# Performance work log

Hardware: AMD Instinct MI355X
Metric: run time of the kernel (lower is better)

Reference implementation:

```python
import jax, jax.numpy as jnp
import numpy as np
import math

EMBED_DIM = 768
NUM_HEADS = 12
HEAD_DIM = EMBED_DIM // NUM_HEADS
EPS = 1e-6


def setup_inputs() -> dict:
    key = jax.random.key(0)
    ks = jax.random.split(key, 9)
    T, B, N, D = 4, 4, 1024, EMBED_DIM
    s = 0.02
    return {
        "x": jax.random.normal(ks[0], (T, B, N, D), dtype=jnp.float32),
        "Wq": jax.random.normal(ks[1], (D, D), dtype=jnp.float32) * s,
        "bq": jax.random.normal(ks[2], (D,), dtype=jnp.float32) * s,
        "Wk": jax.random.normal(ks[3], (D, D), dtype=jnp.float32) * s,
        "bk": jax.random.normal(ks[4], (D,), dtype=jnp.float32) * s,
        "Wv": jax.random.normal(ks[5], (D, D), dtype=jnp.float32) * s,
        "bv": jax.random.normal(ks[6], (D,), dtype=jnp.float32) * s,
        "Wo": jax.random.normal(ks[7], (D, D), dtype=jnp.float32) * s,
        "bo": jax.random.normal(ks[8], (D,), dtype=jnp.float32) * s,
    }


def _split_heads(y, T, B, N):
    # [T,B,N,D] -> [T,B,H,N,Dh]
    return y.reshape(T, B, N, NUM_HEADS, HEAD_DIM).transpose(0, 1, 3, 2, 4)


def reference(x, Wq, bq, Wk, bk, Wv, bv, Wo, bo):
    T, B, N, D = x.shape
    # q/k/v projections (nn.Linear: x @ W^T + b)
    q = _split_heads(x @ Wq.T + bq, T, B, N)
    k = _split_heads(x @ Wk.T + bk, T, B, N)
    v = _split_heads(x @ Wv.T + bv, T, B, N)
    # scores = q k^T / sqrt(head_dim)
    scores = jnp.einsum("tbhnd,tbhmd->tbhnm", q, k) / math.sqrt(HEAD_DIM)
    # spike-form normalization: relu then L1-normalize along keys
    act = jax.nn.relu(scores)
    attn = act / (act.sum(axis=-1, keepdims=True) + EPS)
    ctx = jnp.einsum("tbhnm,tbhmd->tbhnd", attn, v)
    # merge heads: [T,B,H,N,Dh] -> [T,B,N,D]
    out = ctx.transpose(0, 1, 3, 2, 4).reshape(T, B, N, D)
    return out @ Wo.T + bo
```

## Files before the change

### kernel.cpp

```cpp
#include <hip/hip_runtime.h>
#include <hip/hip_bf16.h>
#include <cstdint>


typedef __attribute__((ext_vector_type(8))) short short8;
typedef __attribute__((ext_vector_type(4))) float float4v;
typedef __attribute__((ext_vector_type(16))) float float16v;

__device__ __forceinline__ unsigned short f2bf(float f) {
  unsigned int u = __float_as_uint(f);
  u = (u + 0x7fffu + ((u >> 16) & 1u)) >> 16;
  return (unsigned short)u;
}

__device__ __forceinline__ unsigned int pkbf(float a, float b) {
  unsigned int ua = __float_as_uint(a) + 0x8000u;
  unsigned int ub = __float_as_uint(b) + 0x8000u;
  return __builtin_amdgcn_perm(ub, ua, 0x07060302u);
}

__device__ __forceinline__ void gld_lds16(const void* g, void* lds) {
  __builtin_amdgcn_global_load_lds(
      (__attribute__((address_space(1))) void*)(uintptr_t)g,
      (__attribute__((address_space(3))) void*)(uint32_t)(uintptr_t)lds,
      16, 0, 0);
}

__global__ __launch_bounds__(256) void cast_all(
    const float* __restrict__ x,  const float* __restrict__ Wq,
    const float* __restrict__ Wk, const float* __restrict__ Wv,
    const float* __restrict__ Wo, unsigned short* __restrict__ XBF,
    unsigned short* __restrict__ WQKV, unsigned short* __restrict__ WOb) {
  const int bid = blockIdx.x;
  const float* src;
  unsigned short* dst;
  int i;
  if (bid < 12288) {
    src = x; dst = XBF; i = bid * 256 + threadIdx.x;
  } else {
    const int wb = bid - 12288;
    const int which = wb / 576;
    i = (wb % 576) * 256 + threadIdx.x;
    src = (which == 0) ? Wq : (which == 1) ? Wk : (which == 2) ? Wv : Wo;
    dst = (which == 0) ? WQKV
        : (which == 1) ? WQKV + 589824
        : (which == 2) ? WQKV + 1179648 : WOb;
  }
  float4 f = reinterpret_cast<const float4*>(src)[i];
  ushort4 o;
  o.x = f2bf(f.x); o.y = f2bf(f.y); o.z = f2bf(f.z); o.w = f2bf(f.w);
  reinterpret_cast<ushort4*>(dst)[i] = o;
}

template <bool OUT_BF16>
__global__ __launch_bounds__(256) void gemm_bt(
    const unsigned short* __restrict__ A,
    const unsigned short* __restrict__ Bt,
    unsigned short* __restrict__ Cb,
    float* __restrict__ Cf,
    unsigned short* __restrict__ Vt,
    const float* __restrict__ b0, const float* __restrict__ b1,
    const float* __restrict__ b2, int N) {
  constexpr int K = 768;
  constexpr int KT = K / 32;
  __shared__ unsigned short As[3][128 * 32];
  __shared__ unsigned short Bs[3][128 * 32];

  const int tid = threadIdx.x;
  const int lane = tid & 63;
  const int w = tid >> 6;
  const int wrow = w >> 1, wcol = w & 1;
  const int l15 = lane & 15, quad = lane >> 4;

  const int gx = gridDim.x;
  const int nwg = gx * gridDim.y;
  const int hw = blockIdx.y * gx + blockIdx.x;
  const int per = nwg >> 3;
  const int lg = (hw & 7) * per + (hw >> 3);
  const int bx = lg % gx, by = lg / gx;
  const int i0 = by * 128, j0 = bx * 128;

  const unsigned short* ga = A + (size_t)(i0 + 32 * w + (lane >> 2)) * K + (lane & 3) * 8;
  const unsigned short* gb = Bt + (size_t)(j0 + 32 * w + (lane >> 2)) * K + (lane & 3) * 8;

  auto stage = [&](int kt2, int bufi) {
    const unsigned short* pa = ga + kt2 * 32;
    const unsigned short* pb = gb + kt2 * 32;
    gld_lds16(pa, &As[bufi][(32 * w) * 32]);
    gld_lds16(pa + 16 * K, &As[bufi][(32 * w + 16) * 32]);
    gld_lds16(pb, &Bs[bufi][(32 * w) * 32]);
    gld_lds16(pb + 16 * K, &Bs[bufi][(32 * w + 16) * 32]);
  };

  float4v acc[4][4];
#pragma unroll
  for (int a = 0; a < 4; ++a)
#pragma unroll
    for (int b = 0; b < 4; ++b) acc[a][b] = float4v{0.f, 0.f, 0.f, 0.f};

  stage(0, 0);
  stage(1, 1);
  asm volatile("s_waitcnt vmcnt(4)" ::: "memory");
  __builtin_amdgcn_s_barrier();
  __builtin_amdgcn_sched_barrier(0);

#pragma unroll 1
  for (int kt = 0; kt < KT; ++kt) {
    const int cur = kt % 3;
    if (kt + 2 < KT) stage(kt + 2, (kt + 2) % 3);

    short8 af[4], bfr[4];
#pragma unroll
    for (int a = 0; a < 4; ++a)
      af[a] = *(const short8*)&As[cur][(wrow * 64 + a * 16 + l15) * 32 + quad * 8];
#pragma unroll
    for (int b = 0; b < 4; ++b)
      bfr[b] = *(const short8*)&Bs[cur][(wcol * 64 + b * 16 + l15) * 32 + quad * 8];
#pragma unroll
    for (int a = 0; a < 4; ++a)
#pragma unroll
      for (int b = 0; b < 4; ++b)
        acc[a][b] = __builtin_amdgcn_mfma_f32_16x16x32_bf16(af[a], bfr[b], acc[a][b], 0, 0, 0);

    if (kt + 2 < KT) {
      asm volatile("s_waitcnt vmcnt(4)" ::: "memory");
      __builtin_amdgcn_s_barrier();
      __builtin_amdgcn_sched_barrier(0);
    } else if (kt + 1 < KT) {
      asm volatile("s_waitcnt vmcnt(0)" ::: "memory");
      __builtin_amdgcn_s_barrier();
      __builtin_amdgcn_sched_barrier(0);
    }
  }

  const int sel = j0 / 768;
  const float* bp = (sel == 0) ? b0 : ((sel == 1) ? b1 : b2);
#pragma unroll
  for (int a = 0; a < 4; ++a) {
    const int row0 = i0 + wrow * 64 + a * 16 + quad * 4;
#pragma unroll
    for (int b = 0; b < 4; ++b) {
      const int col = j0 + wcol * 64 + b * 16 + l15;
      const float bias = bp[col - sel * 768];
      if (OUT_BF16 && sel == 2) {
        const int tb = row0 >> 10;
        const int n0 = row0 & 1023;
        const int hd = col - 1536;
        const float v0 = acc[a][b][0] + bias;
        const float v1 = acc[a][b][1] + bias;
        const float v2 = acc[a][b][2] + bias;
        const float v3 = acc[a][b][3] + bias;
        uint2 u;
        u.x = (unsigned int)f2bf(v0) | ((unsigned int)f2bf(v1) << 16);
        u.y = (unsigned int)f2bf(v2) | ((unsigned int)f2bf(v3) << 16);
        *(uint2*)&Vt[((size_t)(tb * 768 + hd)) * 1024 + n0] = u;
      } else {
#pragma unroll
        for (int r = 0; r < 4; ++r) {
          const float v = acc[a][b][r] + bias;
          if (OUT_BF16)
            Cb[(size_t)(row0 + r) * N + col] = f2bf(v);
          else
            Cf[(size_t)(row0 + r) * N + col] = v;
        }
      }
    }
  }
}

__global__ __launch_bounds__(256) void attn32(
    const unsigned short* __restrict__ qkv,
    const unsigned short* __restrict__ vt,
    unsigned short* __restrict__ ctx) {
  __shared__ unsigned short Ks[2][64 * 72];
  __shared__ unsigned short Vs[2][64 * 72];

  const int tbh = blockIdx.x;
  const int qt = blockIdx.y;
  const int tb = tbh / 12, h = tbh % 12;
  const int tid = threadIdx.x, lane = tid & 63, w = tid >> 6;
  const int l31 = lane & 31, hl = lane >> 5;

  short8 qf[2][4];
#pragma unroll
  for (int qs = 0; qs < 2; ++qs) {
    const unsigned short* qp =
        qkv + (size_t)(tb * 1024 + qt * 256 + w * 64 + qs * 32 + l31) * 2304 +
        h * 64 + hl * 8;
#pragma unroll
    for (int kc = 0; kc < 4; ++kc) qf[qs][kc] = *(const short8*)(qp + kc * 16);
  }

  const int srow = tid >> 3;
  const int sblk = tid & 7;
  const unsigned short* kcol =
      qkv + (size_t)(tb * 1024) * 2304 + 768 + h * 64 + sblk * 8;
  const unsigned short* vcol = vt + ((size_t)tbh * 64 + srow) * 1024 + sblk * 8;
  uint4 kr0, kr1, vr0, vr1;
  auto loadKV = [&](int kv) {
    const unsigned short* kp = kcol + (size_t)(kv * 64 + srow) * 2304;
    kr0 = *(const uint4*)kp;
    kr1 = *(const uint4*)(kp + 32 * 2304);
    const unsigned short* vp = vcol + kv * 64;
    vr0 = *(const uint4*)vp;
    vr1 = *(const uint4*)(vp + 32 * 1024);
  };

  float16v octx[2][2];
#pragma unroll
  for (int qs = 0; qs < 2; ++qs)
#pragma unroll
    for (int dt = 0; dt < 2; ++dt)
#pragma unroll
      for (int i = 0; i < 16; ++i) octx[qs][dt][i] = 0.f;
  float den[2] = {0.f, 0.f};

  loadKV(0);

#pragma unroll 1
  for (int kv = 0; kv < 16; ++kv) {
    const int cur = kv & 1;
    *(uint4*)&Ks[cur][srow * 72 + sblk * 8] = kr0;
    *(uint4*)&Ks[cur][(srow + 32) * 72 + sblk * 8] = kr1;
    *(uint4*)&Vs[cur][srow * 72 + sblk * 8] = vr0;
    *(uint4*)&Vs[cur][(srow + 32) * 72 + sblk * 8] = vr1;
    if (kv < 15) loadKV(kv + 1);
    asm volatile("s_waitcnt lgkmcnt(0)" ::: "memory");
    __builtin_amdgcn_s_barrier();
    __builtin_amdgcn_sched_barrier(0);

#pragma unroll
    for (int qs = 0; qs < 2; ++qs) {
      unsigned int pk[2][8];
#pragma unroll
      for (int mt = 0; mt < 2; ++mt) {
        float16v st;
#pragma unroll
        for (int i = 0; i < 16; ++i) st[i] = 0.f;
#pragma unroll
        for (int kc = 0; kc < 4; ++kc) {
          short8 kf =
              *(const short8*)&Ks[cur][(mt * 32 + l31) * 72 + kc * 16 + hl * 8];
          st = __builtin_amdgcn_mfma_f32_32x32x16_bf16(kf, qf[qs][kc], st, 0, 0, 0);
        }
#pragma unroll
        for (int g = 0; g < 4; ++g) {
          float v0 = st[4 * g + 0]; v0 = v0 > 0.f ? v0 : 0.f;
          float v1 = st[4 * g + 1]; v1 = v1 > 0.f ? v1 : 0.f;
          float v2 = st[4 * g + 2]; v2 = v2 > 0.f ? v2 : 0.f;
          float v3 = st[4 * g + 3]; v3 = v3 > 0.f ? v3 : 0.f;
          den[qs] += (v0 + v1) + (v2 + v3);
          pk[mt][g * 2 + 0] = pkbf(v0, v1);
          pk[mt][g * 2 + 1] = pkbf(v2, v3);
        }
      }
#pragma unroll
      for (int kc = 0; kc < 4; ++kc) {
        const int mt = kc >> 1, gb = (kc & 1) * 2;
        unsigned int a0 = pk[mt][gb * 2 + 0], b0 = pk[mt][gb * 2 + 2];
        unsigned int a1 = pk[mt][gb * 2 + 1], b1 = pk[mt][gb * 2 + 3];
        asm("v_permlane32_swap_b32 %0, %1" : "+v"(a0), "+v"(b0));
        asm("v_permlane32_swap_b32 %0, %1" : "+v"(a1), "+v"(b1));
        union { unsigned int u[4]; short8 s; } pf;
        pf.u[0] = a0; pf.u[1] = a1; pf.u[2] = b0; pf.u[3] = b1;
#pragma unroll
        for (int dt = 0; dt < 2; ++dt) {
          short8 vb =
              *(const short8*)&Vs[cur][(dt * 32 + l31) * 72 + kc * 16 + hl * 8];
          octx[qs][dt] = __builtin_amdgcn_mfma_f32_32x32x16_bf16(
              vb, pf.s, octx[qs][dt], 0, 0, 0);
        }
      }
    }
  }

#pragma unroll
  for (int qs = 0; qs < 2; ++qs) {
    float d = den[qs] + __shfl_xor(den[qs], 32);
    const float sc = 1.f / (d + 8e-6f);
    const size_t qrow = (size_t)(tb * 1024 + qt * 256 + w * 64 + qs * 32 + l31);
#pragma unroll
    for (int dt = 0; dt < 2; ++dt)
#pragma unroll
      for (int g = 0; g < 4; ++g) {
        const float v0 = octx[qs][dt][4 * g + 0] * sc;
        const float v1 = octx[qs][dt][4 * g + 1] * sc;
        const float v2 = octx[qs][dt][4 * g + 2] * sc;
        const float v3 = octx[qs][dt][4 * g + 3] * sc;
        uint2 u;
        u.x = pkbf(v0, v1);
        u.y = pkbf(v2, v3);
        *(uint2*)&ctx[qrow * 768 + h * 64 + dt * 32 + g * 8 + hl * 4] = u;
      }
  }
}

extern "C" void kernel_launch(void* const* d_in, const int* in_sizes, int n_in,
                              void* d_out, int out_size, void* d_ws, size_t ws_size,
                              hipStream_t stream) {
  const float* x  = (const float*)d_in[0];
  const float* Wq = (const float*)d_in[1];
  const float* bq = (const float*)d_in[2];
  const float* Wk = (const float*)d_in[3];
  const float* bk = (const float*)d_in[4];
  const float* Wv = (const float*)d_in[5];
  const float* bv = (const float*)d_in[6];
  const float* Wo = (const float*)d_in[7];
  const float* bo = (const float*)d_in[8];
  float* out = (float*)d_out;

  char* ws = (char*)d_ws;
  unsigned short* XBF  = (unsigned short*)(ws);
  unsigned short* CTX  = (unsigned short*)(ws);
  unsigned short* WQKV = (unsigned short*)(ws + 25165824);
  unsigned short* WOb  = (unsigned short*)(ws + 28704768);
  unsigned short* QKV  = (unsigned short*)(ws + 29884416);
  unsigned short* VT   = (unsigned short*)(ws + 105381888);

  cast_all<<<14592, 256, 0, stream>>>(x, Wq, Wk, Wv, Wo, XBF, WQKV, WOb);

  gemm_bt<true><<<dim3(18, 128), 256, 0, stream>>>(XBF, WQKV, QKV, nullptr, VT,
                                                   bq, bk, bv, 2304);
  attn32<<<dim3(192, 4), 256, 0, stream>>>(QKV, VT, CTX);
  gemm_bt<false><<<dim3(6, 128), 256, 0, stream>>>(CTX, WOb, nullptr, out,
                                                   nullptr, bo, bo, bo, 768);
}
```

Before: 303.1 us.

## Use 256x256-tile 8-wave GEMM with interleaved prefetch for QKV projection

Replaces the 128x128-tile QKV projection GEMM with a dedicated 512-thread kernel computing 256x256 tiles. It double-buffers LDS, interleaves per-slice global-to-LDS prefetch with MFMA groups under barriers, and raises wave priority around the MFMA blocks. The larger tiles halve global/LDS traffic per FLOP but use more registers and LDS per block and launch fewer workgroups (576). The output projection GEMM is simplified to a non-templated fp32 variant.

```diff
diff --git a/kernel.cpp b/kernel.cpp
--- a/kernel.cpp
+++ b/kernel.cpp
@@ -52,15 +52,179 @@
   reinterpret_cast<ushort4*>(dst)[i] = o;
 }
 
-template <bool OUT_BF16>
+__global__ __launch_bounds__(512) void gemm256(
+    const unsigned short* __restrict__ A,
+    const unsigned short* __restrict__ Bt,
+    unsigned short* __restrict__ Cb,
+    unsigned short* __restrict__ Vt,
+    const float* __restrict__ b0, const float* __restrict__ b1,
+    const float* __restrict__ b2) {
+  constexpr int K = 768;
+  constexpr int KT = 24;
+  __shared__ unsigned short Ab[2][256 * 32];
+  __shared__ unsigned short Bb[2][256 * 32];
+
+  const int tid = threadIdx.x;
+  const int lane = tid & 63;
+  const int wv = tid >> 6;
+  const int wm = wv >> 2, wn = wv & 3;
+  const int l15 = lane & 15, quad = lane >> 4;
+
+  const int gx = gridDim.x;
+  const int nwg = gx * gridDim.y;
+  const int hw = blockIdx.y * gx + blockIdx.x;
+  const int per = nwg >> 3;
+  const int lg = (hw & 7) * per + (hw >> 3);
+  const int bx = lg % gx, by = lg / gx;
+  const int i0 = by * 256, j0 = bx * 256;
+
+  const int srow = tid >> 2;
+  const int scol = ((tid & 3) << 3) ^ ((srow & 6) << 2);
+  const unsigned short* pa0 = A  + (size_t)(i0 + srow) * K + scol;
+  const unsigned short* pb0 = Bt + (size_t)(j0 + srow) * K + scol;
+  const int xsw = ((quad * 8) ^ ((l15 & 6) * 4));
+  const int aoff = (wm * 128 + l15) * 32 + xsw;
+  const int boff = (wn * 64 + l15) * 32 + xsw;
+
+  auto stA = [&](int kt, int bb, int h) {
+    gld_lds16(pa0 + (size_t)h * 128 * K + kt * 32,
+              &Ab[bb][h * 4096 + wv * 512]);
+  };
+  auto stB = [&](int kt, int bb, int h) {
+    gld_lds16(pb0 + (size_t)h * 128 * K + kt * 32,
+              &Bb[bb][h * 4096 + wv * 512]);
+  };
+
+  float4v acc[8][4];
+#pragma unroll
+  for (int m = 0; m < 8; ++m)
+#pragma unroll
+    for (int n = 0; n < 4; ++n) acc[m][n] = float4v{0.f, 0.f, 0.f, 0.f};
+
+  stB(0, 0, 0); stB(0, 0, 1);
+  stA(0, 0, 0); stA(0, 0, 1);
+  stB(1, 1, 0); stB(1, 1, 1);
+  asm volatile("s_waitcnt vmcnt(2)" ::: "memory");
+  __builtin_amdgcn_s_barrier();
+  __builtin_amdgcn_sched_barrier(0);
+
+#pragma unroll 1
+  for (int t = 0; t < KT; ++t) {
+    const int bb = t & 1, nb = bb ^ 1;
+    short8 bf[4];
+    short8 a0, a1;
+
+#pragma unroll
+    for (int fn = 0; fn < 4; ++fn)
+      bf[fn] = *(const short8*)&Bb[bb][boff + fn * 512];
+    a0 = *(const short8*)&Ab[bb][aoff + 0 * 512];
+    a1 = *(const short8*)&Ab[bb][aoff + 1 * 512];
+    if (t + 1 < KT) stA(t + 1, nb, 0);
+    __builtin_amdgcn_s_barrier();
+    asm volatile("s_waitcnt lgkmcnt(0)" ::: "memory");
+    __builtin_amdgcn_sched_barrier(0);
+    __builtin_amdgcn_s_setprio(1);
+#pragma unroll
+    for (int fn = 0; fn < 4; ++fn)
+      acc[0][fn] = __builtin_amdgcn_mfma_f32_16x16x32_bf16(a0, bf[fn], acc[0][fn], 0, 0, 0);
+#pragma unroll
+    for (int fn = 0; fn < 4; ++fn)
+      acc[1][fn] = __builtin_amdgcn_mfma_f32_16x16x32_bf16(a1, bf[fn], acc[1][fn], 0, 0, 0);
+    __builtin_amdgcn_s_setprio(0);
+    __builtin_amdgcn_s_barrier();
+
+    a0 = *(const short8*)&Ab[bb][aoff + 2 * 512];
+    a1 = *(const short8*)&Ab[bb][aoff + 3 * 512];
+    if (t + 1 < KT) stA(t + 1, nb, 1);
+    __builtin_amdgcn_s_barrier();
+    asm volatile("s_waitcnt lgkmcnt(0)" ::: "memory");
+    __builtin_amdgcn_sched_barrier(0);
+    __builtin_amdgcn_s_setprio(1);
+#pragma unroll
+    for (int fn = 0; fn < 4; ++fn)
+      acc[2][fn] = __builtin_amdgcn_mfma_f32_16x16x32_bf16(a0, bf[fn], acc[2][fn], 0, 0, 0);
+#pragma unroll
+    for (int fn = 0; fn < 4; ++fn)
+      acc[3][fn] = __builtin_amdgcn_mfma_f32_16x16x32_bf16(a1, bf[fn], acc[3][fn], 0, 0, 0);
+    __builtin_amdgcn_s_setprio(0);
+    __builtin_amdgcn_s_barrier();
+
+    a0 = *(const short8*)&Ab[bb][aoff + 4 * 512];
+    a1 = *(const short8*)&Ab[bb][aoff + 5 * 512];
+    if (t + 2 < KT) stB(t + 2, bb, 0);
+    __builtin_amdgcn_s_barrier();
+    asm volatile("s_waitcnt lgkmcnt(0)" ::: "memory");
+    __builtin_amdgcn_sched_barrier(0);
+    __builtin_amdgcn_s_setprio(1);
+#pragma unroll
+    for (int fn = 0; fn < 4; ++fn)
+      acc[4][fn] = __builtin_amdgcn_mfma_f32_16x16x32_bf16(a0, bf[fn], acc[4][fn], 0, 0, 0);
+#pragma unroll
+    for (int fn = 0; fn < 4; ++fn)
+      acc[5][fn] = __builtin_amdgcn_mfma_f32_16x16x32_bf16(a1, bf[fn], acc[5][fn], 0, 0, 0);
+    __builtin_amdgcn_s_setprio(0);
+    __builtin_amdgcn_s_barrier();
+
+    a0 = *(const short8*)&Ab[bb][aoff + 6 * 512];
+    a1 = *(const short8*)&Ab[bb][aoff + 7 * 512];
+    if (t + 2 < KT) stB(t + 2, bb, 1);
+    __builtin_amdgcn_s_barrier();
+    asm volatile("s_waitcnt lgkmcnt(0)" ::: "memory");
+    __builtin_amdgcn_sched_barrier(0);
+    __builtin_amdgcn_s_setprio(1);
+#pragma unroll
+    for (int fn = 0; fn < 4; ++fn)
+      acc[6][fn] = __builtin_amdgcn_mfma_f32_16x16x32_bf16(a0, bf[fn], acc[6][fn], 0, 0, 0);
+#pragma unroll
+    for (int fn = 0; fn < 4; ++fn)
+      acc[7][fn] = __builtin_amdgcn_mfma_f32_16x16x32_bf16(a1, bf[fn], acc[7][fn], 0, 0, 0);
+    __builtin_amdgcn_s_setprio(0);
+    if (t + 2 < KT) {
+      asm volatile("s_waitcnt vmcnt(2)" ::: "memory");
+      __builtin_amdgcn_s_barrier();
+      __builtin_amdgcn_sched_barrier(0);
+    } else if (t + 1 < KT) {
+      asm volatile("s_waitcnt vmcnt(0)" ::: "memory");
+      __builtin_amdgcn_s_barrier();
+      __builtin_amdgcn_sched_barrier(0);
+    }
+  }
+
+  const int sel = bx / 3;
+  const float* bp = (sel == 0) ? b0 : ((sel == 1) ? b1 : b2);
+#pragma unroll
+  for (int fm = 0; fm < 8; ++fm) {
+    const int row0 = i0 + wm * 128 + fm * 16 + quad * 4;
+#pragma unroll
+    for (int fn = 0; fn < 4; ++fn) {
+      const int col = j0 + wn * 64 + fn * 16 + l15;
+      const float bias = bp[col - sel * 768];
+      if (sel == 2) {
+        const int tb = row0 >> 10;
+        const int n0 = row0 & 1023;
+        const int hd = col - 1536;
+        const float v0 = acc[fm][fn][0] + bias;
+        const float v1 = acc[fm][fn][1] + bias;
+        const float v2 = acc[fm][fn][2] + bias;
+        const float v3 = acc[fm][fn][3] + bias;
+        uint2 u;
+        u.x = (unsigned int)f2bf(v0) | ((unsigned int)f2bf(v1) << 16);
+        u.y = (unsigned int)f2bf(v2) | ((unsigned int)f2bf(v3) << 16);
+        *(uint2*)&Vt[((size_t)(tb * 768 + hd)) * 1024 + n0] = u;
+      } else {
+#pragma unroll
+        for (int r = 0; r < 4; ++r)
+          Cb[(size_t)(row0 + r) * 2304 + col] = f2bf(acc[fm][fn][r] + bias);
+      }
+    }
+  }
+}
+
 __global__ __launch_bounds__(256) void gemm_bt(
     const unsigned short* __restrict__ A,
     const unsigned short* __restrict__ Bt,
-    unsigned short* __restrict__ Cb,
     float* __restrict__ Cf,
-    unsigned short* __restrict__ Vt,
-    const float* __restrict__ b0, const float* __restrict__ b1,
-    const float* __restrict__ b2, int N) {
+    const float* __restrict__ b0, int N) {
   constexpr int K = 768;
   constexpr int KT = K / 32;
   __shared__ unsigned short As[3][128 * 32];
@@ -133,37 +297,16 @@
     }
   }
 
-  const int sel = j0 / 768;
-  const float* bp = (sel == 0) ? b0 : ((sel == 1) ? b1 : b2);
 #pragma unroll
   for (int a = 0; a < 4; ++a) {
     const int row0 = i0 + wrow * 64 + a * 16 + quad * 4;
 #pragma unroll
     for (int b = 0; b < 4; ++b) {
       const int col = j0 + wcol * 64 + b * 16 + l15;
-      const float bias = bp[col - sel * 768];
-      if (OUT_BF16 && sel == 2) {
-        const int tb = row0 >> 10;
-        const int n0 = row0 & 1023;
-        const int hd = col - 1536;
-        const float v0 = acc[a][b][0] + bias;
-        const float v1 = acc[a][b][1] + bias;
-        const float v2 = acc[a][b][2] + bias;
-        const float v3 = acc[a][b][3] + bias;
-        uint2 u;
-        u.x = (unsigned int)f2bf(v0) | ((unsigned int)f2bf(v1) << 16);
-        u.y = (unsigned int)f2bf(v2) | ((unsigned int)f2bf(v3) << 16);
-        *(uint2*)&Vt[((size_t)(tb * 768 + hd)) * 1024 + n0] = u;
-      } else {
-#pragma unroll
-        for (int r = 0; r < 4; ++r) {
-          const float v = acc[a][b][r] + bias;
-          if (OUT_BF16)
-            Cb[(size_t)(row0 + r) * N + col] = f2bf(v);
-          else
-            Cf[(size_t)(row0 + r) * N + col] = v;
-        }
-      }
+      const float bias = b0[col];
+#pragma unroll
+      for (int r = 0; r < 4; ++r)
+        Cf[(size_t)(row0 + r) * N + col] = acc[a][b][r] + bias;
     }
   }
 }
@@ -319,9 +462,7 @@
 
   cast_all<<<14592, 256, 0, stream>>>(x, Wq, Wk, Wv, Wo, XBF, WQKV, WOb);
 
-  gemm_bt<true><<<dim3(18, 128), 256, 0, stream>>>(XBF, WQKV, QKV, nullptr, VT,
-                                                   bq, bk, bv, 2304);
+  gemm256<<<dim3(9, 64), 512, 0, stream>>>(XBF, WQKV, QKV, VT, bq, bk, bv);
   attn32<<<dim3(192, 4), 256, 0, stream>>>(QKV, VT, CTX);
-  gemm_bt<false><<<dim3(6, 128), 256, 0, stream>>>(CTX, WOb, nullptr, out,
-                                                   nullptr, bo, bo, bo, 768);
-}
+  gemm_bt<<<dim3(6, 128), 256, 0, stream>>>(CTX, WOb, out, bo, 768);
+}
```

Result: slower. 315.6 us (+4.1%).
